# Kernel optimization log

Measured on AMD Instinct MI355X. Metric: run time of the kernel, lower is better.

## Reference

```python
import jax, jax.numpy as jnp
import numpy as np

B, T, D_IN, H, NEMB = 256, 512, 512, 512, 96


def setup_inputs() -> dict:
    key = jax.random.key(0)
    ks = jax.random.split(key, 12)
    s = 0.02
    return {
        "h": jax.random.normal(ks[0], (B, H), jnp.float32),
        "c": jax.random.normal(ks[1], (B, H), jnp.float32),
        "batch_H": jax.random.normal(ks[2], (B, T, D_IN), jnp.float32),
        "char_onehots": jax.random.uniform(ks[3], (B, NEMB), jnp.float32),
        # i2h: Linear(input_size, hidden, bias=False)
        "Wi2h": jax.random.normal(ks[4], (H, D_IN), jnp.float32) * s,
        # h2h: Linear(hidden, hidden)
        "Wh2h": jax.random.normal(ks[5], (H, H), jnp.float32) * s,
        "bh2h": jax.random.normal(ks[6], (H,), jnp.float32) * s,
        # score: Linear(hidden, 1, bias=False)
        "Wscore": jax.random.normal(ks[7], (1, H), jnp.float32) * s,
        # LSTMCell(input_size + num_embeddings, hidden); pytorch gate order i,f,g,o
        "W_ih": jax.random.normal(ks[8], (4 * H, D_IN + NEMB), jnp.float32) * s,
        "W_hh": jax.random.normal(ks[9], (4 * H, H), jnp.float32) * s,
        "b_ih": jax.random.normal(ks[10], (4 * H,), jnp.float32) * s,
        "b_hh": jax.random.normal(ks[11], (4 * H,), jnp.float32) * s,
    }


def reference(h, c, batch_H, char_onehots, Wi2h, Wh2h, bh2h, Wscore, W_ih, W_hh, b_ih, b_hh):
    # Additive (Bahdanau) attention
    batch_H_proj = jnp.einsum('btd,hd->bth', batch_H, Wi2h)        # [B,T,H]
    prev_hidden_proj = h @ Wh2h.T + bh2h                            # [B,H]
    e = jnp.einsum('bth,oh->bto', jnp.tanh(batch_H_proj + prev_hidden_proj[:, None, :]), Wscore)  # [B,T,1]
    alpha = jax.nn.softmax(e, axis=1)                               # [B,T,1]
    context = jnp.einsum('bt,btd->bd', alpha[..., 0], batch_H)      # [B,D_IN]
    x = jnp.concatenate([context, char_onehots], axis=1)            # [B, D_IN+NEMB]
    # dropout in eval mode = identity (deterministic reference)
    # LSTMCell step (pytorch gate order: i, f, g, o)
    gates = x @ W_ih.T + b_ih + h @ W_hh.T + b_hh                   # [B,4H]
    i_g, f_g, g_g, o_g = jnp.split(gates, 4, axis=1)
    i_g = jax.nn.sigmoid(i_g)
    f_g = jax.nn.sigmoid(f_g)
    g_g = jnp.tanh(g_g)
    o_g = jax.nn.sigmoid(o_g)
    c_new = f_g * c + i_g * g_g
    h_new = o_g * jnp.tanh(c_new)
    return h_new, c_new, alpha
```

## Files before the change

### kernel.cpp

```cpp
#include <hip/hip_runtime.h>
#include <stdint.h>

#define B_    256
#define T_    512
#define DIN   512
#define H_    512
#define NEMB_ 96
#define BT    131072
#define KG    1120

typedef __attribute__((ext_vector_type(8))) short short8;
typedef __attribute__((ext_vector_type(4))) float f32x4;
typedef __attribute__((ext_vector_type(16))) float f32x16;

__device__ __forceinline__ unsigned bf16_rne(float f) {
    unsigned u = __float_as_uint(f);
    return (u + 0x7FFF + ((u >> 16) & 1)) >> 16;
}
__device__ __forceinline__ unsigned pack2(float a, float b) {
    return bf16_rne(a) | (bf16_rne(b) << 16);
}
__device__ __forceinline__ uint4 pack8(float4 f0, float4 f1) {
    uint4 u;
    u.x = pack2(f0.x, f0.y); u.y = pack2(f0.z, f0.w);
    u.z = pack2(f1.x, f1.y); u.w = pack2(f1.z, f1.w);
    return u;
}
__device__ __forceinline__ float tanh_fast(float x) {
    float ex = __expf(2.f * x);
    return 1.f - 2.f / (ex + 1.f);
}
__device__ __forceinline__ float sigmoid_fast(float x) {
    return 1.f / (1.f + __expf(-x));
}

__global__ void k_bswz(const float* __restrict__ W, uint4* __restrict__ Wbf) {
    int u = blockIdx.x * 256 + threadIdx.x;
    int l = u & 63, c = (u >> 6) & 31, nt = u >> 11;
    int row = nt * 32 + (l & 31);
    int k0 = (c * 2 + (l >> 5)) * 8;
    const float4* W4 = (const float4*)(W + (size_t)row * 512 + k0);
    Wbf[u] = pack8(W4[0], W4[1]);
}

__global__ void k_prevproj(const float* __restrict__ hin, const float* __restrict__ Whh,
                           const float* __restrict__ bh, float* __restrict__ pp) {
    __shared__ float hs[512];
    int b = blockIdx.x >> 4, tc = blockIdx.x & 15;
    int tid = threadIdx.x;
    hs[tid]       = hin[b * 512 + tid];
    hs[256 + tid] = hin[b * 512 + 256 + tid];
    __syncthreads();
    int wave = tid >> 6, lane = tid & 63;
    int o = lane >> 3, kg = lane & 7;
    int t = tc * 32 + wave * 8 + o;
    const float4* wr = (const float4*)(Whh + (size_t)t * 512);
    const float4* hv = (const float4*)hs;
    float acc = 0.f;
#pragma unroll
    for (int j = 0; j < 16; ++j) {
        float4 w = wr[j * 8 + kg];
        float4 x = hv[j * 8 + kg];
        acc += w.x * x.x + w.y * x.y + w.z * x.z + w.w * x.w;
    }
#pragma unroll
    for (int off = 1; off < 8; off <<= 1) acc += __shfl_xor(acc, off, 8);
    if (kg == 0) pp[b * 512 + t] = acc + bh[t];
}

__launch_bounds__(512, 4)
__global__ void k_scores(const float* __restrict__ A,
                         const uint4* __restrict__ Wbf,
                         const float* __restrict__ pp,
                         const float* __restrict__ wsc,
                         float* __restrict__ e,
                         float* __restrict__ ctxp,
                         float* __restrict__ sblk)
{
    __shared__ uint4 ldsA[4096];
    __shared__ float es[8][64];
    __shared__ float wts[64];
    __shared__ float pps[512];
    __shared__ float wss[512];
    int tid = threadIdx.x;
    int blockRow = blockIdx.x * 64;
    int b = blockRow >> 9;
    int lane = tid & 63, wave = tid >> 6;
    int l31 = lane & 31, lh = lane >> 5, l7 = lane & 7;

    pps[tid] = pp[b * 512 + tid];
    wss[tid] = wsc[tid];
    const float4* A4 = (const float4*)A;
#pragma unroll
    for (int it = 0; it < 8; ++it) {
        int row = it * 8 + wave;
        size_t gidx = (size_t)(blockRow + row) * 128 + (size_t)lane * 2;
        float4 f0 = A4[gidx], f1 = A4[gidx + 1];
        ldsA[row * 64 + (lane ^ (row & 7))] = pack8(f0, f1);
    }
    __syncthreads();

    const short8* lds8 = (const short8*)ldsA;
    int base0 = l31 * 64;
    int base1 = (32 + l31) * 64;
    const short8* wf = (const short8*)Wbf + wave * 4096 + lane;
    f32x16 aH0T0 = {0.f}, aH0T1 = {0.f}, aH1T0 = {0.f}, aH1T1 = {0.f};
#pragma unroll
    for (int c = 0; c < 32; ++c) {
        int g = c * 2 + lh;
        int gx = g ^ l7;
        short8 a0 = lds8[base0 + gx];
        short8 a1 = lds8[base1 + gx];
        short8 b0 = wf[c * 64];
        short8 b1 = wf[2048 + c * 64];
        aH0T0 = __builtin_amdgcn_mfma_f32_32x32x16_bf16(b0, a0, aH0T0, 0, 0, 0);
        aH0T1 = __builtin_amdgcn_mfma_f32_32x32x16_bf16(b0, a1, aH0T1, 0, 0, 0);
        aH1T0 = __builtin_amdgcn_mfma_f32_32x32x16_bf16(b1, a0, aH1T0, 0, 0, 0);
        aH1T1 = __builtin_amdgcn_mfma_f32_32x32x16_bf16(b1, a1, aH1T1, 0, 0, 0);
    }

    int hb = wave * 64 + 4 * lh;
    float vA = 0.f, vB = 0.f;
#pragma unroll
    for (int r = 0; r < 16; ++r) {
        int h0 = hb + (r & 3) + 8 * (r >> 2);
        float p0 = pps[h0],      w0 = wss[h0];
        float p1 = pps[h0 + 32], w1 = wss[h0 + 32];
        vA += tanh_fast(aH0T0[r] + p0) * w0 + tanh_fast(aH1T0[r] + p1) * w1;
        vB += tanh_fast(aH0T1[r] + p0) * w0 + tanh_fast(aH1T1[r] + p1) * w1;
    }
    vA += __shfl_xor(vA, 32, 64);
    vB += __shfl_xor(vB, 32, 64);
    es[wave][lane] = (lane < 32) ? vA : vB;
    __syncthreads();

    if (tid < 64) {
        float ev = 0.f;
#pragma unroll
        for (int w = 0; w < 8; ++w) ev += es[w][tid];
        e[blockRow + tid] = ev;
        float pexp = __expf(ev);
        wts[tid] = pexp;
        float s = pexp;
#pragma unroll
        for (int off = 1; off < 64; off <<= 1) s += __shfl_xor(s, off, 64);
        if (tid == 0) sblk[blockIdx.x] = s;
    }
    __syncthreads();

    float* part = (float*)ldsA;
    {
        int t0 = wave * 8;
        float4 c0 = {0.f, 0.f, 0.f, 0.f}, c1 = {0.f, 0.f, 0.f, 0.f};
        size_t rb = (size_t)(blockRow + t0) * 128;
#pragma unroll
        for (int i = 0; i < 8; ++i) {
            float wv = wts[t0 + i];
            float4 x0 = A4[rb + (size_t)i * 128 + lane];
            float4 x1 = A4[rb + (size_t)i * 128 + 64 + lane];
            c0.x += wv * x0.x; c0.y += wv * x0.y; c0.z += wv * x0.z; c0.w += wv * x0.w;
            c1.x += wv * x1.x; c1.y += wv * x1.y; c1.z += wv * x1.z; c1.w += wv * x1.w;
        }
        ((float4*)part)[wave * 128 + lane]      = c0;
        ((float4*)part)[wave * 128 + 64 + lane] = c1;
    }
    __syncthreads();
    {
        float s = 0.f;
#pragma unroll
        for (int w = 0; w < 8; ++w) s += part[w * 512 + tid];
        ctxp[(size_t)blockIdx.x * 512 + tid] = s;
    }
}

__global__ void k_alpha(const float* __restrict__ sblk, float* __restrict__ ealpha,
                        float* __restrict__ invd) {
    int i = blockIdx.x * 256 + threadIdx.x;
    int b = i >> 9;
    const float* sb = sblk + b * 8;
    float s = (sb[0] + sb[1]) + (sb[2] + sb[3]) + (sb[4] + sb[5]) + (sb[6] + sb[7]);
    float inv = 1.f / s;
    ealpha[i] = __expf(ealpha[i]) * inv;
    if ((i & 511) == 0) invd[b] = inv;
}

__global__ void k_xcat(const float* __restrict__ ctxp, const float* __restrict__ invd,
                       const float* __restrict__ oneh, const float* __restrict__ hin,
                       uint4* __restrict__ xbf) {
    int u = blockIdx.x * 256 + threadIdx.x;
    int l = u & 63, r = u >> 6;
    int c = r % 70, bt = r / 70;
    int row = bt * 32 + (l & 31);
    int k0 = (c * 2 + (l >> 5)) * 8;
    float4 f0, f1;
    if (k0 < 512) {
        const float4* p4 = (const float4*)(ctxp + (size_t)row * 4096 + k0);
        float4 a = {0.f, 0.f, 0.f, 0.f}, bq = {0.f, 0.f, 0.f, 0.f};
#pragma unroll
        for (int q = 0; q < 8; ++q) {
            float4 s0 = p4[q * 128];
            float4 s1 = p4[q * 128 + 1];
            a.x += s0.x;  a.y += s0.y;  a.z += s0.z;  a.w += s0.w;
            bq.x += s1.x; bq.y += s1.y; bq.z += s1.z; bq.w += s1.w;
        }
        float inv = invd[row];
        f0.x = a.x * inv;  f0.y = a.y * inv;  f0.z = a.z * inv;  f0.w = a.w * inv;
        f1.x = bq.x * inv; f1.y = bq.y * inv; f1.z = bq.z * inv; f1.w = bq.w * inv;
    } else if (k0 < 608) {
        const float4* s4 = (const float4*)(oneh + (size_t)row * 96 + (k0 - 512));
        f0 = s4[0]; f1 = s4[1];
    } else {
        const float4* s4 = (const float4*)(hin + (size_t)row * 512 + (k0 - 608));
        f0 = s4[0]; f1 = s4[1];
    }
    xbf[u] = pack8(f0, f1);
}

__global__ void k_wcat(const float* __restrict__ Wih, const float* __restrict__ Whh,
                       uint4* __restrict__ wgf) {
    int u = blockIdx.x * 256 + threadIdx.x;
    int l = u & 63, r = u >> 6;
    int c = r % 70, gt = r / 70;
    int g = gt * 32 + (l & 31);
    int k0 = (c * 2 + (l >> 5)) * 8;
    const float4* s4;
    if (k0 < 608) s4 = (const float4*)(Wih + (size_t)g * 608 + k0);
    else          s4 = (const float4*)(Whh + (size_t)g * 512 + (k0 - 608));
    wgf[u] = pack8(s4[0], s4[1]);
}

__launch_bounds__(256, 4)
__global__ void k_gates(const uint4* __restrict__ xbf,
                        const uint4* __restrict__ wgf,
                        float* __restrict__ gates5) {
    int tid = threadIdx.x;
    int lane = tid & 63, wave = tid >> 6;
    int l31 = lane & 31, lh = lane >> 5;
    int wid = blockIdx.x * 4 + wave;
    int gI = wid & 63, bI = (wid >> 6) & 7, kI = wid >> 9;

    const short8* ax = (const short8*)xbf + (size_t)(bI * 70 + kI * 14) * 64 + lane;
    const short8* bx = (const short8*)wgf + (size_t)(gI * 70 + kI * 14) * 64 + lane;

    f32x16 acc = {0.f};
#pragma unroll
    for (int c = 0; c < 14; ++c) {
        short8 a = ax[c * 64];
        short8 b = bx[c * 64];
        acc = __builtin_amdgcn_mfma_f32_32x32x16_bf16(a, b, acc, 0, 0, 0);
    }
    float* gout = gates5 + (size_t)kI * (B_ * 2048)
                + (size_t)(bI * 32 + 4 * lh) * 2048 + gI * 32 + l31;
#pragma unroll
    for (int r = 0; r < 16; ++r)
        gout[(size_t)((r & 3) + 8 * (r >> 2)) * 2048] = acc[r];
}

__global__ void k_lstm(const float* __restrict__ gates5, const float* __restrict__ c,
                       const float* __restrict__ bih, const float* __restrict__ bhh,
                       float* __restrict__ out) {
    int i = blockIdx.x * 256 + threadIdx.x;
    int b = i >> 9, u = i & 511;
    size_t base = (size_t)b * 2048 + u;
    float gi = bih[u]        + bhh[u];
    float gf = bih[512 + u]  + bhh[512 + u];
    float gg = bih[1024 + u] + bhh[1024 + u];
    float go = bih[1536 + u] + bhh[1536 + u];
#pragma unroll
    for (int s = 0; s < 5; ++s) {
        const float* g = gates5 + (size_t)s * (B_ * 2048) + base;
        gi += g[0]; gf += g[512]; gg += g[1024]; go += g[1536];
    }
    float si = sigmoid_fast(gi);
    float sf = sigmoid_fast(gf);
    float tg = tanh_fast(gg);
    float so = sigmoid_fast(go);
    float cn = sf * c[i] + si * tg;
    float hn = so * tanh_fast(cn);
    out[i] = hn;
    out[BT + i] = cn;
}

extern "C" void kernel_launch(void* const* d_in, const int* in_sizes, int n_in,
                              void* d_out, int out_size, void* d_ws, size_t ws_size,
                              hipStream_t stream) {
    const float* hin  = (const float*)d_in[0];
    const float* c    = (const float*)d_in[1];
    const float* bH   = (const float*)d_in[2];
    const float* oneh = (const float*)d_in[3];
    const float* Wi2h = (const float*)d_in[4];
    const float* Wh2h = (const float*)d_in[5];
    const float* bh2h = (const float*)d_in[6];
    const float* Wsc  = (const float*)d_in[7];
    const float* Wih  = (const float*)d_in[8];
    const float* Whh  = (const float*)d_in[9];
    const float* bih  = (const float*)d_in[10];
    const float* bhh  = (const float*)d_in[11];
    float* out = (float*)d_out;
    float* alpha = out + 2 * BT;

    char* w = (char*)d_ws;
    uint4* xbf    = (uint4*)w;
    uint4* wgf    = (uint4*)(w + 573440);
    uint4* Wbf    = (uint4*)(w + 5160960);
    float* pp     = (float*)(w + 5685248);
    float* ctxp   = (float*)(w + 6209536);
    float* sblk   = (float*)(w + 10403840);
    float* invd   = (float*)(w + 10412032);
    float* gates5 = (float*)(w + 5160960);

    k_bswz    <<<128, 256, 0, stream>>>(Wi2h, Wbf);
    k_wcat    <<<1120, 256, 0, stream>>>(Wih, Whh, wgf);
    k_prevproj<<<4096, 256, 0, stream>>>(hin, Wh2h, bh2h, pp);
    k_scores  <<<2048, 512, 0, stream>>>(bH, Wbf, pp, Wsc, alpha, ctxp, sblk);
    k_alpha   <<<512, 256, 0, stream>>>(sblk, alpha, invd);
    k_xcat    <<<140, 256, 0, stream>>>(ctxp, invd, oneh, hin, xbf);
    k_gates   <<<640, 256, 0, stream>>>(xbf, wgf, gates5);
    k_lstm    <<<512, 256, 0, stream>>>(gates5, c, bih, bhh, out);
}
```

Before: 495.6 us.

## Software-pipeline k_scores over 256-row tiles with double-buffered LDS K-halves

Each k_scores block now handles 256 timesteps (four 64-row tiles) in eight K-half stages. The next stage's global loads go to registers while MFMAs run on the current LDS buffer, so load latency overlaps with compute. Context partials stay in registers across tiles, which cuts the ctxp partials from 8 to 2 per batch and simplifies k_xcat and k_alpha. The trade-off is that the grid shrinks from 2048 to 512 blocks, which lowers parallelism and adds extra barriers per stage.

```diff
diff --git a/kernel.cpp b/kernel.cpp
--- a/kernel.cpp
+++ b/kernel.cpp
@@ -77,108 +77,139 @@
                          float* __restrict__ ctxp,
                          float* __restrict__ sblk)
 {
-    __shared__ uint4 ldsA[4096];
+    __shared__ uint4 buf[2][2048];
     __shared__ float es[8][64];
-    __shared__ float wts[64];
     __shared__ float pps[512];
     __shared__ float wss[512];
     int tid = threadIdx.x;
-    int blockRow = blockIdx.x * 64;
-    int b = blockRow >> 9;
     int lane = tid & 63, wave = tid >> 6;
     int l31 = lane & 31, lh = lane >> 5, l7 = lane & 7;
+    int b = blockIdx.x >> 1;
+    int R0 = blockIdx.x * 256;
 
     pps[tid] = pp[b * 512 + tid];
     wss[tid] = wsc[tid];
+
     const float4* A4 = (const float4*)A;
-#pragma unroll
-    for (int it = 0; it < 8; ++it) {
-        int row = it * 8 + wave;
-        size_t gidx = (size_t)(blockRow + row) * 128 + (size_t)lane * 2;
-        float4 f0 = A4[gidx], f1 = A4[gidx + 1];
-        ldsA[row * 64 + (lane ^ (row & 7))] = pack8(f0, f1);
-    }
+    int srow = wave * 2 + (lane >> 5);
+    int sk8  = lane & 31;
+
+    float4 L[8];
+#pragma unroll
+    for (int it = 0; it < 4; ++it) {
+        size_t gi = (size_t)(R0 + it * 16 + srow) * 128 + (size_t)sk8 * 2;
+        L[2 * it] = A4[gi]; L[2 * it + 1] = A4[gi + 1];
+    }
+#pragma unroll
+    for (int it = 0; it < 4; ++it) {
+        int row = it * 16 + srow;
+        buf[0][row * 32 + (sk8 ^ (row & 7))] = pack8(L[2 * it], L[2 * it + 1]);
+    }
+
+    const short8* wfb = (const short8*)Wbf + wave * 4096 + lane;
+    f32x16 a00, a01, a10, a11;
+#pragma unroll
+    for (int r = 0; r < 16; ++r) { a00[r] = 0.f; a01[r] = 0.f; a10[r] = 0.f; a11[r] = 0.f; }
+    float4 c0 = {0.f, 0.f, 0.f, 0.f}, c1 = {0.f, 0.f, 0.f, 0.f};
+    float ssum = 0.f;
+
+    for (int i = 0; i < 8; ++i) {
+        int kh = i & 1;
+        if (i < 7) {
+            int s2 = (i + 1) >> 1, kh2 = (i + 1) & 1;
+#pragma unroll
+            for (int it = 0; it < 4; ++it) {
+                size_t gi = (size_t)(R0 + s2 * 64 + it * 16 + srow) * 128
+                          + (size_t)(kh2 * 64) + (size_t)sk8 * 2;
+                L[2 * it] = A4[gi]; L[2 * it + 1] = A4[gi + 1];
+            }
+        }
+        __syncthreads();
+
+        const short8* lds8 = (const short8*)buf[i & 1];
+        int base0 = l31 * 32, base1 = (32 + l31) * 32;
+        const short8* wf = wfb + kh * 1024;
+#pragma unroll
+        for (int c = 0; c < 16; ++c) {
+            int gx = (c * 2 + lh) ^ l7;
+            short8 x0 = lds8[base0 + gx];
+            short8 x1 = lds8[base1 + gx];
+            short8 w0 = wf[c * 64];
+            short8 w1 = wf[2048 + c * 64];
+            a00 = __builtin_amdgcn_mfma_f32_32x32x16_bf16(w0, x0, a00, 0, 0, 0);
+            a01 = __builtin_amdgcn_mfma_f32_32x32x16_bf16(w0, x1, a01, 0, 0, 0);
+            a10 = __builtin_amdgcn_mfma_f32_32x32x16_bf16(w1, x0, a10, 0, 0, 0);
+            a11 = __builtin_amdgcn_mfma_f32_32x32x16_bf16(w1, x1, a11, 0, 0, 0);
+        }
+
+        if (kh == 1) {
+            int s = i >> 1;
+            int hb = wave * 64 + 4 * lh;
+            float vA = 0.f, vB = 0.f;
+#pragma unroll
+            for (int r = 0; r < 16; ++r) {
+                int h0 = hb + (r & 3) + 8 * (r >> 2);
+                float p0 = pps[h0],      w0s = wss[h0];
+                float p1 = pps[h0 + 32], w1s = wss[h0 + 32];
+                vA += tanh_fast(a00[r] + p0) * w0s + tanh_fast(a10[r] + p1) * w1s;
+                vB += tanh_fast(a01[r] + p0) * w0s + tanh_fast(a11[r] + p1) * w1s;
+            }
+            vA += __shfl_xor(vA, 32, 64);
+            vB += __shfl_xor(vB, 32, 64);
+            es[wave][lane] = (lane < 32) ? vA : vB;
+#pragma unroll
+            for (int r = 0; r < 16; ++r) { a00[r] = 0.f; a01[r] = 0.f; a10[r] = 0.f; a11[r] = 0.f; }
+            __syncthreads();
+
+            float ev = 0.f;
+#pragma unroll
+            for (int w = 0; w < 8; ++w) ev += es[w][lane];
+            float wtv = __expf(ev);
+            if (wave == 0) {
+                e[R0 + s * 64 + lane] = ev;
+                float ss = wtv;
+#pragma unroll
+                for (int off = 1; off < 64; off <<= 1) ss += __shfl_xor(ss, off, 64);
+                ssum += ss;
+            }
+            size_t rb = (size_t)(R0 + s * 64 + wave * 8) * 128;
+#pragma unroll
+            for (int j = 0; j < 8; ++j) {
+                float wv = __shfl(wtv, wave * 8 + j, 64);
+                float4 x0 = A4[rb + (size_t)j * 128 + lane];
+                float4 x1 = A4[rb + (size_t)j * 128 + 64 + lane];
+                c0.x += wv * x0.x; c0.y += wv * x0.y; c0.z += wv * x0.z; c0.w += wv * x0.w;
+                c1.x += wv * x1.x; c1.y += wv * x1.y; c1.z += wv * x1.z; c1.w += wv * x1.w;
+            }
+        }
+
+        __syncthreads();
+        if (i < 7) {
+            int nb = (i + 1) & 1;
+#pragma unroll
+            for (int it = 0; it < 4; ++it) {
+                int row = it * 16 + srow;
+                buf[nb][row * 32 + (sk8 ^ (row & 7))] = pack8(L[2 * it], L[2 * it + 1]);
+            }
+        }
+    }
+
+    float* part = (float*)buf;
+    ((float4*)part)[wave * 128 + lane]      = c0;
+    ((float4*)part)[wave * 128 + 64 + lane] = c1;
     __syncthreads();
-
-    const short8* lds8 = (const short8*)ldsA;
-    int base0 = l31 * 64;
-    int base1 = (32 + l31) * 64;
-    const short8* wf = (const short8*)Wbf + wave * 4096 + lane;
-    f32x16 aH0T0 = {0.f}, aH0T1 = {0.f}, aH1T0 = {0.f}, aH1T1 = {0.f};
-#pragma unroll
-    for (int c = 0; c < 32; ++c) {
-        int g = c * 2 + lh;
-        int gx = g ^ l7;
-        short8 a0 = lds8[base0 + gx];
-        short8 a1 = lds8[base1 + gx];
-        short8 b0 = wf[c * 64];
-        short8 b1 = wf[2048 + c * 64];
-        aH0T0 = __builtin_amdgcn_mfma_f32_32x32x16_bf16(b0, a0, aH0T0, 0, 0, 0);
-        aH0T1 = __builtin_amdgcn_mfma_f32_32x32x16_bf16(b0, a1, aH0T1, 0, 0, 0);
-        aH1T0 = __builtin_amdgcn_mfma_f32_32x32x16_bf16(b1, a0, aH1T0, 0, 0, 0);
-        aH1T1 = __builtin_amdgcn_mfma_f32_32x32x16_bf16(b1, a1, aH1T1, 0, 0, 0);
-    }
-
-    int hb = wave * 64 + 4 * lh;
-    float vA = 0.f, vB = 0.f;
-#pragma unroll
-    for (int r = 0; r < 16; ++r) {
-        int h0 = hb + (r & 3) + 8 * (r >> 2);
-        float p0 = pps[h0],      w0 = wss[h0];
-        float p1 = pps[h0 + 32], w1 = wss[h0 + 32];
-        vA += tanh_fast(aH0T0[r] + p0) * w0 + tanh_fast(aH1T0[r] + p1) * w1;
-        vB += tanh_fast(aH0T1[r] + p0) * w0 + tanh_fast(aH1T1[r] + p1) * w1;
-    }
-    vA += __shfl_xor(vA, 32, 64);
-    vB += __shfl_xor(vB, 32, 64);
-    es[wave][lane] = (lane < 32) ? vA : vB;
-    __syncthreads();
-
-    if (tid < 64) {
-        float ev = 0.f;
-#pragma unroll
-        for (int w = 0; w < 8; ++w) ev += es[w][tid];
-        e[blockRow + tid] = ev;
-        float pexp = __expf(ev);
-        wts[tid] = pexp;
-        float s = pexp;
-#pragma unroll
-        for (int off = 1; off < 64; off <<= 1) s += __shfl_xor(s, off, 64);
-        if (tid == 0) sblk[blockIdx.x] = s;
-    }
-    __syncthreads();
-
-    float* part = (float*)ldsA;
-    {
-        int t0 = wave * 8;
-        float4 c0 = {0.f, 0.f, 0.f, 0.f}, c1 = {0.f, 0.f, 0.f, 0.f};
-        size_t rb = (size_t)(blockRow + t0) * 128;
-#pragma unroll
-        for (int i = 0; i < 8; ++i) {
-            float wv = wts[t0 + i];
-            float4 x0 = A4[rb + (size_t)i * 128 + lane];
-            float4 x1 = A4[rb + (size_t)i * 128 + 64 + lane];
-            c0.x += wv * x0.x; c0.y += wv * x0.y; c0.z += wv * x0.z; c0.w += wv * x0.w;
-            c1.x += wv * x1.x; c1.y += wv * x1.y; c1.z += wv * x1.z; c1.w += wv * x1.w;
-        }
-        ((float4*)part)[wave * 128 + lane]      = c0;
-        ((float4*)part)[wave * 128 + 64 + lane] = c1;
-    }
-    __syncthreads();
-    {
-        float s = 0.f;
-#pragma unroll
-        for (int w = 0; w < 8; ++w) s += part[w * 512 + tid];
-        ctxp[(size_t)blockIdx.x * 512 + tid] = s;
-    }
+    float s = 0.f;
+#pragma unroll
+    for (int w = 0; w < 8; ++w) s += part[w * 512 + tid];
+    ctxp[(size_t)blockIdx.x * 512 + tid] = s;
+    if (tid == 0) sblk[blockIdx.x] = ssum;
 }
 
 __global__ void k_alpha(const float* __restrict__ sblk, float* __restrict__ ealpha,
                         float* __restrict__ invd) {
     int i = blockIdx.x * 256 + threadIdx.x;
     int b = i >> 9;
-    const float* sb = sblk + b * 8;
-    float s = (sb[0] + sb[1]) + (sb[2] + sb[3]) + (sb[4] + sb[5]) + (sb[6] + sb[7]);
+    float s = sblk[b * 2] + sblk[b * 2 + 1];
     float inv = 1.f / s;
     ealpha[i] = __expf(ealpha[i]) * inv;
     if ((i & 511) == 0) invd[b] = inv;
@@ -194,18 +225,14 @@
     int k0 = (c * 2 + (l >> 5)) * 8;
     float4 f0, f1;
     if (k0 < 512) {
-        const float4* p4 = (const float4*)(ctxp + (size_t)row * 4096 + k0);
-        float4 a = {0.f, 0.f, 0.f, 0.f}, bq = {0.f, 0.f, 0.f, 0.f};
-#pragma unroll
-        for (int q = 0; q < 8; ++q) {
-            float4 s0 = p4[q * 128];
-            float4 s1 = p4[q * 128 + 1];
-            a.x += s0.x;  a.y += s0.y;  a.z += s0.z;  a.w += s0.w;
-            bq.x += s1.x; bq.y += s1.y; bq.z += s1.z; bq.w += s1.w;
-        }
+        const float4* p4 = (const float4*)(ctxp + (size_t)row * 1024 + k0);
+        float4 s0 = p4[0],   s1 = p4[1];
+        float4 t0 = p4[128], t1 = p4[129];
         float inv = invd[row];
-        f0.x = a.x * inv;  f0.y = a.y * inv;  f0.z = a.z * inv;  f0.w = a.w * inv;
-        f1.x = bq.x * inv; f1.y = bq.y * inv; f1.z = bq.z * inv; f1.w = bq.w * inv;
+        f0.x = (s0.x + t0.x) * inv; f0.y = (s0.y + t0.y) * inv;
+        f0.z = (s0.z + t0.z) * inv; f0.w = (s0.w + t0.w) * inv;
+        f1.x = (s1.x + t1.x) * inv; f1.y = (s1.y + t1.y) * inv;
+        f1.z = (s1.z + t1.z) * inv; f1.w = (s1.w + t1.w) * inv;
     } else if (k0 < 608) {
         const float4* s4 = (const float4*)(oneh + (size_t)row * 96 + (k0 - 512));
         f0 = s4[0]; f1 = s4[1];
@@ -312,7 +339,7 @@
     k_bswz    <<<128, 256, 0, stream>>>(Wi2h, Wbf);
     k_wcat    <<<1120, 256, 0, stream>>>(Wih, Whh, wgf);
     k_prevproj<<<4096, 256, 0, stream>>>(hin, Wh2h, bh2h, pp);
-    k_scores  <<<2048, 512, 0, stream>>>(bH, Wbf, pp, Wsc, alpha, ctxp, sblk);
+    k_scores  <<<512, 512, 0, stream>>>(bH, Wbf, pp, Wsc, alpha, ctxp, sblk);
     k_alpha   <<<512, 256, 0, stream>>>(sblk, alpha, invd);
     k_xcat    <<<140, 256, 0, stream>>>(ctxp, invd, oneh, hin, xbf);
     k_gates   <<<640, 256, 0, stream>>>(xbf, wgf, gates5);
```

Measured after the change: 605.7 us. +22.2%, slower.
